# Performance work log

Measured on AMD Instinct MI355X. Metric: run time of the kernel, lower is better.

Reference implementation:

```python
import jax, jax.numpy as jnp
import numpy as np

NUM_HEAD = 12
D_MODEL = 768
SEQ_LEN = 4096
D_K = D_MODEL // NUM_HEAD
NEG = -1e9  # matches masked_fill(-1000000000.0)


def setup_inputs() -> dict:
    key = jax.random.key(0)
    ks = jax.random.split(key, 9)
    s = 1.0 / np.sqrt(D_MODEL)
    inp = {
        "x": jax.random.normal(ks[0], (1, SEQ_LEN, D_MODEL), jnp.float32),
        "Wq": jax.random.normal(ks[1], (D_MODEL, D_MODEL), jnp.float32) * s,
        "bq": jax.random.normal(ks[2], (D_MODEL,), jnp.float32) * 0.01,
        "Wk": jax.random.normal(ks[3], (D_MODEL, D_MODEL), jnp.float32) * s,
        "bk": jax.random.normal(ks[4], (D_MODEL,), jnp.float32) * 0.01,
        "Wv": jax.random.normal(ks[5], (D_MODEL, D_MODEL), jnp.float32) * s,
        "bv": jax.random.normal(ks[6], (D_MODEL,), jnp.float32) * 0.01,
        "Wo": jax.random.normal(ks[7], (D_MODEL, D_MODEL), jnp.float32) * s,
        "bo": jax.random.normal(ks[8], (D_MODEL,), jnp.float32) * 0.01,
    }
    return inp


def reference(x, Wq, bq, Wk, bk, Wv, bv, Wo, bo):
    # x: [B, S, D]. nn.Linear computes x @ W.T + b.
    B, S, D = x.shape

    def proj(W, b):
        y = jnp.einsum("bsd,ed->bse", x, W) + b
        # [B, S, H, d_k] -> [B, H, S, d_k]
        return y.reshape(B, S, NUM_HEAD, D_K).transpose(0, 2, 1, 3)

    q = proj(Wq, bq)
    k = proj(Wk, bk)
    v = proj(Wv, bv)

    scores = jnp.einsum("bhqd,bhkd->bhqk", q, k) / jnp.sqrt(
        jnp.asarray(D_K, x.dtype)
    )
    # causal (subsequent) mask: position q attends to k <= q
    causal = jnp.tril(jnp.ones((S, S), bool))
    scores = jnp.where(causal[None, None], scores, jnp.asarray(NEG, x.dtype))
    p_attn = jax.nn.softmax(scores, axis=-1)  # dropout is identity in eval
    ctx = jnp.einsum("bhqk,bhkd->bhqd", p_attn, v)
    ctx = ctx.transpose(0, 2, 1, 3).reshape(B, S, D)
    return jnp.einsum("bsd,ed->bse", ctx, Wo) + bo
```

## Files before the change

### kernel.cpp

```cpp
#include <hip/hip_runtime.h>

#define SEQ 4096
#define DM  768
#define NH  12
#define DK  64

typedef __bf16 bf16_t;
typedef bf16_t bf16x8 __attribute__((ext_vector_type(8)));
typedef bf16_t bf16x4 __attribute__((ext_vector_type(4)));
typedef float  f32x4  __attribute__((ext_vector_type(4)));
typedef short  s16x4  __attribute__((ext_vector_type(4)));

#define LOG2E 1.44269504088896340736f
#define SM_C2 23.0831207f

static __device__ inline f32x4 mfma16x16x16_bf16(bf16x4 a, bf16x4 b, f32x4 c) {
#if __has_builtin(__builtin_amdgcn_mfma_f32_16x16x16_bf16)
    return __builtin_amdgcn_mfma_f32_16x16x16_bf16(a, b, c, 0, 0, 0);
#else
    return __builtin_amdgcn_mfma_f32_16x16x16bf16_1k(
        __builtin_bit_cast(s16x4, a), __builtin_bit_cast(s16x4, b), c, 0, 0, 0);
#endif
}

static __device__ __forceinline__ void gl_lds16(const bf16_t* g, bf16_t* l) {
    __builtin_amdgcn_global_load_lds(
        (const __attribute__((address_space(1))) void*)g,
        (__attribute__((address_space(3))) void*)l, 16, 0, 0);
}

__global__ __launch_bounds__(256) void cvt_bf16(
    const float* __restrict__ x,  const float* __restrict__ Wq,
    const float* __restrict__ Wk, const float* __restrict__ Wv,
    const float* __restrict__ Wo,
    bf16_t* __restrict__ xb, bf16_t* __restrict__ Wb)
{
    const int NXV = SEQ * DM / 4;
    const int NWV = DM * DM / 4;
    int i4 = blockIdx.x * 256 + threadIdx.x;
    const float* src; bf16_t* dst; int off;
    if (i4 < NXV) { src = x; dst = xb; off = i4; }
    else {
        int j = i4 - NXV;
        int w = j / NWV, jj = j - w * NWV;
        src = (w == 0) ? Wq : (w == 1) ? Wk : (w == 2) ? Wv : Wo;
        dst = Wb + (size_t)w * DM * DM;
        off = jj;
    }
    float4 v = *(const float4*)&src[(size_t)off * 4];
    bf16x4 t;
    t[0] = (bf16_t)v.x; t[1] = (bf16_t)v.y; t[2] = (bf16_t)v.z; t[3] = (bf16_t)v.w;
    *(bf16x4*)&dst[(size_t)off * 4] = t;
}

__global__ __launch_bounds__(256) void gemm_qkv2(
    const bf16_t* __restrict__ A, const bf16_t* __restrict__ Wb,
    const float* __restrict__ bq, const float* __restrict__ bk,
    const float* __restrict__ bv,
    bf16_t* __restrict__ Qb, bf16_t* __restrict__ Kb, bf16_t* __restrict__ Vbt)
{
    const int z = blockIdx.z;
    const bf16_t* W = Wb + (size_t)z * DM * DM;
    const float* bias = (z == 0) ? bq : (z == 1) ? bk : bv;

    __shared__ bf16_t As[128][64];
    __shared__ bf16_t Bs[128][64];

    const int tid  = threadIdx.x;
    const int wave = tid >> 6;
    const int lane = tid & 63;
    const int wm   = wave & 1, wn = wave >> 1;
    const int lrow = lane & 15;
    const int quad = lane >> 4;
    const int row0 = blockIdx.x * 128;
    const int col0 = blockIdx.y * 128;

    const int srow   = lane >> 3;
    const int schunk = (lane & 7) ^ srow;
    const int swz    = lrow & 7;

    f32x4 acc[4][4];
    #pragma unroll
    for (int i = 0; i < 4; i++)
        #pragma unroll
        for (int j = 0; j < 4; j++)
            acc[i][j] = (f32x4){0.f, 0.f, 0.f, 0.f};

    for (int k0 = 0; k0 < DM; k0 += 64) {
        __syncthreads();
        #pragma unroll
        for (int u = 0; u < 4; u++) {
            int R0 = wave * 32 + u * 8;
            gl_lds16(&A[(size_t)(row0 + R0 + srow) * DM + k0 + schunk * 8],
                     &As[R0][0]);
            gl_lds16(&W[(size_t)(col0 + R0 + srow) * DM + k0 + schunk * 8],
                     &Bs[R0][0]);
        }
        __syncthreads();

        #pragma unroll
        for (int s = 0; s < 2; s++) {
            bf16x8 af[4], bfr[4];
            #pragma unroll
            for (int mt = 0; mt < 4; mt++)
                af[mt] = *(const bf16x8*)
                    &As[wm * 64 + mt * 16 + lrow][(((s << 2) | quad) ^ swz) * 8];
            #pragma unroll
            for (int nt = 0; nt < 4; nt++)
                bfr[nt] = *(const bf16x8*)
                    &Bs[wn * 64 + nt * 16 + lrow][(((s << 2) | quad) ^ swz) * 8];
            #pragma unroll
            for (int mt = 0; mt < 4; mt++)
                #pragma unroll
                for (int nt = 0; nt < 4; nt++)
                    acc[mt][nt] = __builtin_amdgcn_mfma_f32_16x16x32_bf16(
                        af[mt], bfr[nt], acc[mt][nt], 0, 0, 0);
        }
    }

    if (z == 2) {
        #pragma unroll
        for (int nt = 0; nt < 4; nt++) {
            int col = col0 + wn * 64 + nt * 16 + lrow;
            float bvv = bias[col];
            #pragma unroll
            for (int mt = 0; mt < 4; mt++) {
                int row = row0 + wm * 64 + mt * 16 + quad * 4;
                bf16x4 t;
                #pragma unroll
                for (int r = 0; r < 4; r++) t[r] = (bf16_t)(acc[mt][nt][r] + bvv);
                *(bf16x4*)&Vbt[(size_t)col * SEQ + row] = t;
            }
        }
    } else {
        bf16_t* Cout = (z == 0) ? Qb : Kb;
        float scale = (z == 1) ? (0.125f * LOG2E) : 1.0f;
        #pragma unroll
        for (int nt = 0; nt < 4; nt++) {
            int col = col0 + wn * 64 + nt * 16 + lrow;
            float bvv = bias[col];
            #pragma unroll
            for (int mt = 0; mt < 4; mt++) {
                #pragma unroll
                for (int r = 0; r < 4; r++) {
                    int row = row0 + wm * 64 + mt * 16 + quad * 4 + r;
                    Cout[(size_t)row * DM + col] =
                        (bf16_t)((acc[mt][nt][r] + bvv) * scale);
                }
            }
        }
    }
}

__global__ __launch_bounds__(256) void gemm_out2(
    const bf16_t* __restrict__ A, const bf16_t* __restrict__ W,
    const float* __restrict__ bias, float* __restrict__ C)
{
    __shared__ bf16_t As[128][64];
    __shared__ bf16_t Bs[64][64];

    const int tid  = threadIdx.x;
    const int wave = tid >> 6;
    const int lane = tid & 63;
    const int wm   = wave & 1, wn = wave >> 1;
    const int lrow = lane & 15;
    const int quad = lane >> 4;
    const int row0 = blockIdx.x * 128;
    const int col0 = blockIdx.y * 64;

    const int srow   = lane >> 3;
    const int schunk = (lane & 7) ^ srow;
    const int swz    = lrow & 7;

    f32x4 acc[4][2];
    #pragma unroll
    for (int i = 0; i < 4; i++)
        #pragma unroll
        for (int j = 0; j < 2; j++)
            acc[i][j] = (f32x4){0.f, 0.f, 0.f, 0.f};

    for (int k0 = 0; k0 < DM; k0 += 64) {
        __syncthreads();
        #pragma unroll
        for (int u = 0; u < 4; u++) {
            int R0 = wave * 32 + u * 8;
            gl_lds16(&A[(size_t)(row0 + R0 + srow) * DM + k0 + schunk * 8],
                     &As[R0][0]);
        }
        #pragma unroll
        for (int u = 0; u < 2; u++) {
            int R0 = wave * 16 + u * 8;
            gl_lds16(&W[(size_t)(col0 + R0 + srow) * DM + k0 + schunk * 8],
                     &Bs[R0][0]);
        }
        __syncthreads();

        #pragma unroll
        for (int s = 0; s < 2; s++) {
            bf16x8 af[4], bfr[2];
            #pragma unroll
            for (int mt = 0; mt < 4; mt++)
                af[mt] = *(const bf16x8*)
                    &As[wm * 64 + mt * 16 + lrow][(((s << 2) | quad) ^ swz) * 8];
            #pragma unroll
            for (int nt = 0; nt < 2; nt++)
                bfr[nt] = *(const bf16x8*)
                    &Bs[wn * 32 + nt * 16 + lrow][(((s << 2) | quad) ^ swz) * 8];
            #pragma unroll
            for (int mt = 0; mt < 4; mt++)
                #pragma unroll
                for (int nt = 0; nt < 2; nt++)
                    acc[mt][nt] = __builtin_amdgcn_mfma_f32_16x16x32_bf16(
                        af[mt], bfr[nt], acc[mt][nt], 0, 0, 0);
        }
    }

    #pragma unroll
    for (int nt = 0; nt < 2; nt++) {
        int col = col0 + wn * 32 + nt * 16 + lrow;
        float bvv = bias[col];
        #pragma unroll
        for (int mt = 0; mt < 4; mt++) {
            #pragma unroll
            for (int r = 0; r < 4; r++) {
                int row = row0 + wm * 64 + mt * 16 + quad * 4 + r;
                C[(size_t)row * DM + col] = acc[mt][nt][r] + bvv;
            }
        }
    }
}

__global__ __launch_bounds__(512) void flash_split3(
    const bf16_t* __restrict__ Qb, const bf16_t* __restrict__ Kb,
    const bf16_t* __restrict__ Vbt,
    float* __restrict__ Oacc ,
    float* __restrict__ Lacc )
{
    const int h = blockIdx.z;
    const int f = blockIdx.x;
    int g = 0;
    while (f >= 2 * (g + 1) * (g + 2)) g++;
    const int rem = f - 2 * g * (g + 1);
    const int qs  = rem / (g + 1);
    const int seg = rem - qs * (g + 1);
    const int qi  = g * 4 + qs;
    const int q0  = qi << 7;
    const int kt0    = seg << 3;
    const int ktlast = min(kt0 + 7, 2 * qi + 1);

    const int tid  = threadIdx.x;
    const int wave = tid >> 6;
    const int lane = tid & 63;
    const int lrow = lane & 15;
    const int quad = lane >> 4;
    const int swz  = lrow & 7;

    __shared__ bf16_t Ks[2][64][64];
    __shared__ bf16_t Vs[2][64][64];

    const int qrow = q0 + wave * 16 + lrow;
    bf16x8 qfrag[2];
    #pragma unroll
    for (int s = 0; s < 2; s++)
        qfrag[s] = *(const bf16x8*)&Qb[(size_t)qrow * DM + h * DK + s * 32 + quad * 8];

    f32x4 oT[4];
    #pragma unroll
    for (int dt = 0; dt < 4; dt++) oT[dt] = (f32x4){0.f, 0.f, 0.f, 0.f};
    float l_i = 0.f;

    const int sr  = tid >> 3;
    const int sc0 = tid & 7;
    const int scn = sc0 ^ (sr & 7);
    const bf16_t* Kbase = Kb  + (size_t)h * DK;
    const bf16_t* Vbase = Vbt + (size_t)(h * DK) * SEQ;

    size_t ko = (size_t)kt0 << 6;
    bf16x8 kr = *(const bf16x8*)&Kbase[(ko + sr) * DM + sc0 * 8];
    bf16x8 vr = *(const bf16x8*)&Vbase[(size_t)sr * SEQ + ko + sc0 * 8];

    for (int kt = kt0; kt <= ktlast; kt++) {
        const int b = kt & 1;
        *(bf16x8*)&Ks[b][sr][scn * 8] = kr;
        *(bf16x8*)&Vs[b][sr][scn * 8] = vr;
        __syncthreads();

        if (kt < ktlast) {
            size_t kn = (size_t)(kt + 1) << 6;
            kr = *(const bf16x8*)&Kbase[(kn + sr) * DM + sc0 * 8];
            vr = *(const bf16x8*)&Vbase[(size_t)sr * SEQ + kn + sc0 * 8];
        }

        if ((kt << 6) > q0 + wave * 16 + 15) continue;

        f32x4 sc[4];
        #pragma unroll
        for (int mt = 0; mt < 4; mt++) {
            f32x4 a = (f32x4){0.f, 0.f, 0.f, 0.f};
            #pragma unroll
            for (int s = 0; s < 2; s++) {
                bf16x8 kf = *(const bf16x8*)
                    &Ks[b][mt * 16 + lrow][((((s << 2) | quad)) ^ swz) * 8];
                a = __builtin_amdgcn_mfma_f32_16x16x32_bf16(kf, qfrag[s], a, 0, 0, 0);
            }
            sc[mt] = a;
        }

        if ((kt << 6) + 63 > q0 + wave * 16) {
            #pragma unroll
            for (int mt = 0; mt < 4; mt++)
                #pragma unroll
                for (int rr = 0; rr < 4; rr++)
                    if ((kt << 6) + mt * 16 + quad * 4 + rr > qrow)
                        sc[mt][rr] = -1e30f;
        }

        bf16x4 pf[4];
        float rsum = 0.f;
        #pragma unroll
        for (int mt = 0; mt < 4; mt++) {
            bf16x4 t;
            #pragma unroll
            for (int rr = 0; rr < 4; rr++) {
                float p = __builtin_amdgcn_exp2f(sc[mt][rr] - SM_C2);
                rsum += p;
                t[rr] = (bf16_t)p;
            }
            pf[mt] = t;
        }
        l_i += rsum;

        #pragma unroll
        for (int dt = 0; dt < 4; dt++)
            #pragma unroll
            for (int kb = 0; kb < 4; kb++) {
                int c16 = (kb * 2 + (quad >> 1)) ^ swz;
                bf16x4 vf = *(const bf16x4*)
                    &Vs[b][dt * 16 + lrow][c16 * 8 + (quad & 1) * 4];
                oT[dt] = mfma16x16x16_bf16(vf, pf[kb], oT[dt]);
            }
    }

    #pragma unroll
    for (int dt = 0; dt < 4; dt++)
        #pragma unroll
        for (int rr = 0; rr < 4; rr++) {
            int d = dt * 16 + quad * 4 + rr;
            atomicAdd(&Oacc[((size_t)h * DK + d) * SEQ + qrow], oT[dt][rr]);
        }
    l_i += __shfl_xor(l_i, 16, 64);
    l_i += __shfl_xor(l_i, 32, 64);
    if (quad == 0)
        atomicAdd(&Lacc[(size_t)h * SEQ + qrow], l_i);
}

__global__ __launch_bounds__(256) void ctx_epilogue(
    const float* __restrict__ Oacc, const float* __restrict__ Lacc,
    bf16_t* __restrict__ Ctx)
{
    const int qt = blockIdx.x;
    const int h  = blockIdx.y;
    const int tid = threadIdx.x;
    __shared__ float T[64][65];

    #pragma unroll
    for (int i = 0; i < 4; i++) {
        int v  = tid + i * 256;
        int d  = v >> 4;
        int qv = v & 15;
        f32x4 o4 = *(const f32x4*)&Oacc[((size_t)h * DK + d) * SEQ + qt * 64 + qv * 4];
        f32x4 l4 = *(const f32x4*)&Lacc[(size_t)h * SEQ + qt * 64 + qv * 4];
        #pragma unroll
        for (int j = 0; j < 4; j++)
            T[qv * 4 + j][d] = o4[j] / l4[j];
    }
    __syncthreads();
    #pragma unroll
    for (int i = 0; i < 2; i++) {
        int v  = tid + i * 256;
        int q  = v >> 3;
        int c8 = v & 7;
        bf16x8 t;
        #pragma unroll
        for (int j = 0; j < 8; j++)
            t[j] = (bf16_t)T[q][c8 * 8 + j];
        *(bf16x8*)&Ctx[(size_t)(qt * 64 + q) * DM + h * DK + c8 * 8] = t;
    }
}

extern "C" void kernel_launch(void* const* d_in, const int* in_sizes, int n_in,
                              void* d_out, int out_size, void* d_ws, size_t ws_size,
                              hipStream_t stream) {
    const float* x  = (const float*)d_in[0];
    const float* Wq = (const float*)d_in[1];
    const float* bq = (const float*)d_in[2];
    const float* Wk = (const float*)d_in[3];
    const float* bk = (const float*)d_in[4];
    const float* Wv = (const float*)d_in[5];
    const float* bv = (const float*)d_in[6];
    const float* Wo = (const float*)d_in[7];
    const float* bo = (const float*)d_in[8];
    float* out = (float*)d_out;

    const size_t NX = (size_t)SEQ * DM;
    const size_t NW = (size_t)DM * DM;

    bf16_t* xb   = (bf16_t*)d_ws;
    bf16_t* Qb   = xb  + NX;
    bf16_t* Kb   = Qb  + NX;
    bf16_t* Vbt  = Kb  + NX;
    bf16_t* Wb   = Vbt + NX;
    float*  Oacc = (float*)(Wb + 4 * NW);
    float*  Lacc = Oacc + NX;
    bf16_t* Cx   = xb;

    int cvt_blocks = (int)((NX + 4 * NW) / 4 / 256);
    cvt_bf16<<<cvt_blocks, 256, 0, stream>>>(x, Wq, Wk, Wv, Wo, xb, Wb);
    hipMemsetAsync(Oacc, 0, (NX + (size_t)NH * SEQ) * 4, stream);

    dim3 g1(SEQ / 128, DM / 128, 3);
    gemm_qkv2<<<g1, 256, 0, stream>>>(xb, Wb, bq, bk, bv, Qb, Kb, Vbt);

    dim3 g2(144, 1, NH);
    flash_split3<<<g2, 512, 0, stream>>>(Qb, Kb, Vbt, Oacc, Lacc);

    dim3 g3(SEQ / 64, NH);
    ctx_epilogue<<<g3, 256, 0, stream>>>(Oacc, Lacc, Cx);

    dim3 g4(SEQ / 128, DM / 64);
    gemm_out2<<<g4, 256, 0, stream>>>(Cx, Wb + 3 * NW, bo, out);
}
```

Baseline: 204.1 us.

## Give each attention wave two query tiles and stage K/V straight into LDS

The split-K flash kernel goes from 512 threads to 256. Each of the four waves now handles 32 query rows as two 16-row tiles, so every K and V fragment read from LDS feeds two MFMAs instead of one. K/V staging no longer passes through registers before an LDS store; it uses direct global-to-LDS copies (gl_lds16) into the double buffer, issued right after the barrier. This is meant to cut LDS read traffic and register staging cost, at the price of more accumulator registers per wave and fewer waves per block to hide latency.

```diff
diff --git a/kernel.cpp b/kernel.cpp
--- a/kernel.cpp
+++ b/kernel.cpp
@@ -230,7 +230,7 @@
     }
 }
 
-__global__ __launch_bounds__(512) void flash_split3(
+__global__ __launch_bounds__(256, 4) void flash_split4(
     const bf16_t* __restrict__ Qb, const bf16_t* __restrict__ Kb,
     const bf16_t* __restrict__ Vbt,
     float* __restrict__ Oacc ,
@@ -258,77 +258,121 @@
     __shared__ bf16_t Ks[2][64][64];
     __shared__ bf16_t Vs[2][64][64];
 
-    const int qrow = q0 + wave * 16 + lrow;
-    bf16x8 qfrag[2];
-    #pragma unroll
-    for (int s = 0; s < 2; s++)
-        qfrag[s] = *(const bf16x8*)&Qb[(size_t)qrow * DM + h * DK + s * 32 + quad * 8];
-
-    f32x4 oT[4];
-    #pragma unroll
-    for (int dt = 0; dt < 4; dt++) oT[dt] = (f32x4){0.f, 0.f, 0.f, 0.f};
-    float l_i = 0.f;
-
-    const int sr  = tid >> 3;
-    const int sc0 = tid & 7;
-    const int scn = sc0 ^ (sr & 7);
-    const bf16_t* Kbase = Kb  + (size_t)h * DK;
-    const bf16_t* Vbase = Vbt + (size_t)(h * DK) * SEQ;
-
-    size_t ko = (size_t)kt0 << 6;
-    bf16x8 kr = *(const bf16x8*)&Kbase[(ko + sr) * DM + sc0 * 8];
-    bf16x8 vr = *(const bf16x8*)&Vbase[(size_t)sr * SEQ + ko + sc0 * 8];
+    const int rbase = q0 + wave * 32;
+    bf16x8 qf[2][2];
+    #pragma unroll
+    for (int c = 0; c < 2; c++)
+        #pragma unroll
+        for (int s = 0; s < 2; s++)
+            qf[c][s] = *(const bf16x8*)
+                &Qb[(size_t)(rbase + c * 16 + lrow) * DM + h * DK + s * 32 + quad * 8];
+
+    f32x4 oT0[4], oT1[4];
+    #pragma unroll
+    for (int dt = 0; dt < 4; dt++) {
+        oT0[dt] = (f32x4){0.f, 0.f, 0.f, 0.f};
+        oT1[dt] = (f32x4){0.f, 0.f, 0.f, 0.f};
+    }
+    float l0 = 0.f, l1 = 0.f;
+
+    const int srow8 = lane >> 3;
+    const int schnk = (lane & 7) ^ srow8;
+
+    #define STAGE(bb, kk)                                                      \
+        do {                                                                   \
+            size_t ko_ = (size_t)(kk) << 6;                                    \
+            _Pragma("unroll")                                                  \
+            for (int r_ = 0; r_ < 2; r_++) {                                   \
+                int row_ = wave * 16 + r_ * 8;                                 \
+                gl_lds16(&Kb[(ko_ + row_ + srow8) * DM + h * DK + schnk * 8],  \
+                         &Ks[bb][row_][0]);                                    \
+                gl_lds16(&Vbt[(size_t)(h * DK + row_ + srow8) * SEQ + ko_ +    \
+                              schnk * 8],                                      \
+                         &Vs[bb][row_][0]);                                    \
+            }                                                                  \
+        } while (0)
+
+    STAGE(0, kt0);
 
     for (int kt = kt0; kt <= ktlast; kt++) {
         const int b = kt & 1;
-        *(bf16x8*)&Ks[b][sr][scn * 8] = kr;
-        *(bf16x8*)&Vs[b][sr][scn * 8] = vr;
         __syncthreads();
-
-        if (kt < ktlast) {
-            size_t kn = (size_t)(kt + 1) << 6;
-            kr = *(const bf16x8*)&Kbase[(kn + sr) * DM + sc0 * 8];
-            vr = *(const bf16x8*)&Vbase[(size_t)sr * SEQ + kn + sc0 * 8];
-        }
-
-        if ((kt << 6) > q0 + wave * 16 + 15) continue;
-
-        f32x4 sc[4];
+        if (kt < ktlast) STAGE(b ^ 1, kt + 1);
+
+        const int kbase = kt << 6;
+        const bool a0 = (kbase <= rbase + 15);
+        const bool a1 = (kbase <= rbase + 31);
+        if (!a1) continue;
+
+        f32x4 s0[4], s1[4];
         #pragma unroll
         for (int mt = 0; mt < 4; mt++) {
-            f32x4 a = (f32x4){0.f, 0.f, 0.f, 0.f};
-            #pragma unroll
-            for (int s = 0; s < 2; s++) {
+            s0[mt] = (f32x4){0.f, 0.f, 0.f, 0.f};
+            s1[mt] = (f32x4){0.f, 0.f, 0.f, 0.f};
+        }
+        #pragma unroll
+        for (int s = 0; s < 2; s++)
+            #pragma unroll
+            for (int mt = 0; mt < 4; mt++) {
                 bf16x8 kf = *(const bf16x8*)
-                    &Ks[b][mt * 16 + lrow][((((s << 2) | quad)) ^ swz) * 8];
-                a = __builtin_amdgcn_mfma_f32_16x16x32_bf16(kf, qfrag[s], a, 0, 0, 0);
-            }
-            sc[mt] = a;
-        }
-
-        if ((kt << 6) + 63 > q0 + wave * 16) {
+                    &Ks[b][mt * 16 + lrow][(((s << 2) | quad) ^ swz) * 8];
+                if (a0)
+                    s0[mt] = __builtin_amdgcn_mfma_f32_16x16x32_bf16(
+                        kf, qf[0][s], s0[mt], 0, 0, 0);
+                s1[mt] = __builtin_amdgcn_mfma_f32_16x16x32_bf16(
+                    kf, qf[1][s], s1[mt], 0, 0, 0);
+            }
+
+        if (kbase + 63 > rbase) {
+            int qg0 = rbase + lrow;
             #pragma unroll
             for (int mt = 0; mt < 4; mt++)
                 #pragma unroll
                 for (int rr = 0; rr < 4; rr++)
-                    if ((kt << 6) + mt * 16 + quad * 4 + rr > qrow)
-                        sc[mt][rr] = -1e30f;
-        }
-
-        bf16x4 pf[4];
-        float rsum = 0.f;
-        #pragma unroll
-        for (int mt = 0; mt < 4; mt++) {
-            bf16x4 t;
-            #pragma unroll
-            for (int rr = 0; rr < 4; rr++) {
-                float p = __builtin_amdgcn_exp2f(sc[mt][rr] - SM_C2);
-                rsum += p;
-                t[rr] = (bf16_t)p;
-            }
-            pf[mt] = t;
-        }
-        l_i += rsum;
+                    if (kbase + mt * 16 + quad * 4 + rr > qg0)
+                        s0[mt][rr] = -1e30f;
+        }
+        if (kbase + 63 > rbase + 16) {
+            int qg1 = rbase + 16 + lrow;
+            #pragma unroll
+            for (int mt = 0; mt < 4; mt++)
+                #pragma unroll
+                for (int rr = 0; rr < 4; rr++)
+                    if (kbase + mt * 16 + quad * 4 + rr > qg1)
+                        s1[mt][rr] = -1e30f;
+        }
+
+        bf16x4 pf0[4], pf1[4];
+        if (a0) {
+            float rsum = 0.f;
+            #pragma unroll
+            for (int mt = 0; mt < 4; mt++) {
+                bf16x4 t;
+                #pragma unroll
+                for (int rr = 0; rr < 4; rr++) {
+                    float p = __builtin_amdgcn_exp2f(s0[mt][rr] - SM_C2);
+                    rsum += p;
+                    t[rr] = (bf16_t)p;
+                }
+                pf0[mt] = t;
+            }
+            l0 += rsum;
+        }
+        {
+            float rsum = 0.f;
+            #pragma unroll
+            for (int mt = 0; mt < 4; mt++) {
+                bf16x4 t;
+                #pragma unroll
+                for (int rr = 0; rr < 4; rr++) {
+                    float p = __builtin_amdgcn_exp2f(s1[mt][rr] - SM_C2);
+                    rsum += p;
+                    t[rr] = (bf16_t)p;
+                }
+                pf1[mt] = t;
+            }
+            l1 += rsum;
+        }
 
         #pragma unroll
         for (int dt = 0; dt < 4; dt++)
@@ -337,21 +381,30 @@
                 int c16 = (kb * 2 + (quad >> 1)) ^ swz;
                 bf16x4 vf = *(const bf16x4*)
                     &Vs[b][dt * 16 + lrow][c16 * 8 + (quad & 1) * 4];
-                oT[dt] = mfma16x16x16_bf16(vf, pf[kb], oT[dt]);
-            }
-    }
+                if (a0) oT0[dt] = mfma16x16x16_bf16(vf, pf0[kb], oT0[dt]);
+                oT1[dt] = mfma16x16x16_bf16(vf, pf1[kb], oT1[dt]);
+            }
+    }
+    #undef STAGE
 
     #pragma unroll
     for (int dt = 0; dt < 4; dt++)
         #pragma unroll
         for (int rr = 0; rr < 4; rr++) {
             int d = dt * 16 + quad * 4 + rr;
-            atomicAdd(&Oacc[((size_t)h * DK + d) * SEQ + qrow], oT[dt][rr]);
-        }
-    l_i += __shfl_xor(l_i, 16, 64);
-    l_i += __shfl_xor(l_i, 32, 64);
-    if (quad == 0)
-        atomicAdd(&Lacc[(size_t)h * SEQ + qrow], l_i);
+            atomicAdd(&Oacc[((size_t)h * DK + d) * SEQ + rbase + lrow],
+                      oT0[dt][rr]);
+            atomicAdd(&Oacc[((size_t)h * DK + d) * SEQ + rbase + 16 + lrow],
+                      oT1[dt][rr]);
+        }
+    l0 += __shfl_xor(l0, 16, 64);
+    l0 += __shfl_xor(l0, 32, 64);
+    l1 += __shfl_xor(l1, 16, 64);
+    l1 += __shfl_xor(l1, 32, 64);
+    if (quad == 0) {
+        atomicAdd(&Lacc[(size_t)h * SEQ + rbase + lrow], l0);
+        atomicAdd(&Lacc[(size_t)h * SEQ + rbase + 16 + lrow], l1);
+    }
 }
 
 __global__ __launch_bounds__(256) void ctx_epilogue(
@@ -422,7 +475,7 @@
     gemm_qkv2<<<g1, 256, 0, stream>>>(xb, Wb, bq, bk, bv, Qb, Kb, Vbt);
 
     dim3 g2(144, 1, NH);
-    flash_split3<<<g2, 512, 0, stream>>>(Qb, Kb, Vbt, Oacc, Lacc);
+    flash_split4<<<g2, 256, 0, stream>>>(Qb, Kb, Vbt, Oacc, Lacc);
 
     dim3 g3(SEQ / 64, NH);
     ctx_epilogue<<<g3, 256, 0, stream>>>(Oacc, Lacc, Cx);
```

After: 463.9 us. 2.27x slower.

## Split flash attention into 64-row query blocks with 256 threads, heaviest-first order

Applied to the files above, without the earlier changes.

Query tiles in the split flash kernel shrink from 128 to 64 rows, giving 4 waves per block instead of 8. The grid doubles to 288 blocks per head, and blocks are issued in reverse so the longest causal segments start first. Each thread now loads two K/V rows per tile, and the per-wave early-skip is replaced by masking only on the diagonal tile. This aims at better load balance and occupancy, at the cost of more K/V reloads per query row and more atomic partial-sum traffic.

```diff
diff --git a/kernel.cpp b/kernel.cpp
--- a/kernel.cpp
+++ b/kernel.cpp
@@ -230,23 +230,23 @@
     }
 }
 
-__global__ __launch_bounds__(512) void flash_split3(
+__global__ __launch_bounds__(256) void flash_split5(
     const bf16_t* __restrict__ Qb, const bf16_t* __restrict__ Kb,
     const bf16_t* __restrict__ Vbt,
     float* __restrict__ Oacc ,
     float* __restrict__ Lacc )
 {
     const int h = blockIdx.z;
-    const int f = blockIdx.x;
+    const int f = 287 - blockIdx.x;
     int g = 0;
-    while (f >= 2 * (g + 1) * (g + 2)) g++;
-    const int rem = f - 2 * g * (g + 1);
+    while (f >= 4 * (g + 1) * (g + 2)) g++;
+    const int rem = f - 4 * g * (g + 1);
     const int qs  = rem / (g + 1);
     const int seg = rem - qs * (g + 1);
-    const int qi  = g * 4 + qs;
-    const int q0  = qi << 7;
+    const int qi  = g * 8 + qs;
+    const int q0  = qi << 6;
     const int kt0    = seg << 3;
-    const int ktlast = min(kt0 + 7, 2 * qi + 1);
+    const int ktlast = min(kt0 + 7, qi);
 
     const int tid  = threadIdx.x;
     const int wave = tid >> 6;
@@ -269,29 +269,33 @@
     for (int dt = 0; dt < 4; dt++) oT[dt] = (f32x4){0.f, 0.f, 0.f, 0.f};
     float l_i = 0.f;
 
-    const int sr  = tid >> 3;
-    const int sc0 = tid & 7;
-    const int scn = sc0 ^ (sr & 7);
-    const bf16_t* Kbase = Kb  + (size_t)h * DK;
-    const bf16_t* Vbase = Vbt + (size_t)(h * DK) * SEQ;
+    const int r0  = tid >> 3;
+    const int c0  = tid & 7;
+    const int sk0 = c0 ^ (r0 & 7);
+    const bf16_t* Kbase = Kb  + (size_t)h * DK + c0 * 8;
+    const bf16_t* Vbase = Vbt + (size_t)(h * DK) * SEQ + c0 * 8;
 
     size_t ko = (size_t)kt0 << 6;
-    bf16x8 kr = *(const bf16x8*)&Kbase[(ko + sr) * DM + sc0 * 8];
-    bf16x8 vr = *(const bf16x8*)&Vbase[(size_t)sr * SEQ + ko + sc0 * 8];
+    bf16x8 kr0 = *(const bf16x8*)&Kbase[(ko + r0)      * DM];
+    bf16x8 kr1 = *(const bf16x8*)&Kbase[(ko + r0 + 32) * DM];
+    bf16x8 vr0 = *(const bf16x8*)&Vbase[(size_t)(r0)      * SEQ + ko];
+    bf16x8 vr1 = *(const bf16x8*)&Vbase[(size_t)(r0 + 32) * SEQ + ko];
 
     for (int kt = kt0; kt <= ktlast; kt++) {
         const int b = kt & 1;
-        *(bf16x8*)&Ks[b][sr][scn * 8] = kr;
-        *(bf16x8*)&Vs[b][sr][scn * 8] = vr;
+        *(bf16x8*)&Ks[b][r0][sk0 * 8]      = kr0;
+        *(bf16x8*)&Ks[b][r0 + 32][sk0 * 8] = kr1;
+        *(bf16x8*)&Vs[b][r0][sk0 * 8]      = vr0;
+        *(bf16x8*)&Vs[b][r0 + 32][sk0 * 8] = vr1;
         __syncthreads();
 
         if (kt < ktlast) {
             size_t kn = (size_t)(kt + 1) << 6;
-            kr = *(const bf16x8*)&Kbase[(kn + sr) * DM + sc0 * 8];
-            vr = *(const bf16x8*)&Vbase[(size_t)sr * SEQ + kn + sc0 * 8];
-        }
-
-        if ((kt << 6) > q0 + wave * 16 + 15) continue;
+            kr0 = *(const bf16x8*)&Kbase[(kn + r0)      * DM];
+            kr1 = *(const bf16x8*)&Kbase[(kn + r0 + 32) * DM];
+            vr0 = *(const bf16x8*)&Vbase[(size_t)(r0)      * SEQ + kn];
+            vr1 = *(const bf16x8*)&Vbase[(size_t)(r0 + 32) * SEQ + kn];
+        }
 
         f32x4 sc[4];
         #pragma unroll
@@ -300,13 +304,13 @@
             #pragma unroll
             for (int s = 0; s < 2; s++) {
                 bf16x8 kf = *(const bf16x8*)
-                    &Ks[b][mt * 16 + lrow][((((s << 2) | quad)) ^ swz) * 8];
+                    &Ks[b][mt * 16 + lrow][(((s << 2) | quad) ^ swz) * 8];
                 a = __builtin_amdgcn_mfma_f32_16x16x32_bf16(kf, qfrag[s], a, 0, 0, 0);
             }
             sc[mt] = a;
         }
 
-        if ((kt << 6) + 63 > q0 + wave * 16) {
+        if (kt == qi) {
             #pragma unroll
             for (int mt = 0; mt < 4; mt++)
                 #pragma unroll
@@ -421,8 +425,8 @@
     dim3 g1(SEQ / 128, DM / 128, 3);
     gemm_qkv2<<<g1, 256, 0, stream>>>(xb, Wb, bq, bk, bv, Qb, Kb, Vbt);
 
-    dim3 g2(144, 1, NH);
-    flash_split3<<<g2, 512, 0, stream>>>(Qb, Kb, Vbt, Oacc, Lacc);
+    dim3 g2(288, 1, NH);
+    flash_split5<<<g2, 256, 0, stream>>>(Qb, Kb, Vbt, Oacc, Lacc);
 
     dim3 g3(SEQ / 64, NH);
     ctx_epilogue<<<g3, 256, 0, stream>>>(Oacc, Lacc, Cx);
```

Result: no change. 204.0 us (-0.0%).
